# Performance work log

Hardware: AMD Instinct MI355X
Metric: run time of the kernel (lower is better)

The kernel has to match this reference:

```python
import jax, jax.numpy as jnp
import numpy as np

B, T, S0 = 8, 4, 4096
D_MODEL, H, D, R, RANK = 2048, 16, 128, 64, 512
C = D - R  # content dim = 64


def _rope(x, positions):
    # x: [B, H, T, R]; rotate-half style RoPE as in the torch module
    half = x.shape[-1] // 2
    inv_freq = 1.0 / (10000.0 ** (jnp.arange(half, dtype=jnp.float32) / half))
    freqs = positions.astype(jnp.float32)[:, None] * inv_freq[None, :]  # [T, half]
    cos = jnp.cos(freqs)[None, None].astype(x.dtype)
    sin = jnp.sin(freqs)[None, None].astype(x.dtype)
    x1, x2 = x[..., :half], x[..., half:]
    return jnp.concatenate([x1 * cos - x2 * sin, x1 * sin + x2 * cos], axis=-1)


def setup_inputs() -> dict:
    key = jax.random.key(0)
    ks = jax.random.split(key, 9)
    s = 0.02
    return {
        "x": jax.random.normal(ks[0], (B, T, D_MODEL), jnp.float32),
        "cache_c_kv": jax.random.normal(ks[1], (B, S0, RANK), jnp.float32),
        "cache_k_rope": jax.random.normal(ks[2], (B, S0, H, R), jnp.float32),
        "w_q": jax.random.normal(ks[3], (D_MODEL, H * C), jnp.float32) * s,
        "w_q_rope": jax.random.normal(ks[4], (D_MODEL, H * R), jnp.float32) * s,
        "w_kv_down": jax.random.normal(ks[5], (D_MODEL, RANK), jnp.float32) * s,
        "w_kv_up": jax.random.normal(ks[6], (RANK, H * D), jnp.float32) * s,
        "w_k_rope": jax.random.normal(ks[7], (D_MODEL, H * R), jnp.float32) * s,
        "w_out": jax.random.normal(ks[8], (H * D, D_MODEL), jnp.float32) * s,
    }


def reference(x, cache_c_kv, cache_k_rope, w_q, w_q_rope, w_kv_down, w_kv_up, w_k_rope, w_out):
    cache_len = cache_c_kv.shape[1]
    positions = jnp.arange(cache_len, cache_len + T)

    # queries
    q_content = (x @ w_q).reshape(B, T, H, C).transpose(0, 2, 1, 3)        # [B,H,T,C]
    q_rope = (x @ w_q_rope).reshape(B, T, H, R).transpose(0, 2, 1, 3)      # [B,H,T,R]
    q_rope = _rope(q_rope, positions)
    q = jnp.concatenate([q_content, q_rope], axis=-1)                       # [B,H,T,D]

    # new compressed kv + rope keys, append to cache
    c_kv_new = x @ w_kv_down                                                # [B,T,RANK]
    k_rope_new = (x @ w_k_rope).reshape(B, T, H, R).transpose(0, 2, 1, 3)
    k_rope_new = _rope(k_rope_new, positions).transpose(0, 2, 1, 3)         # [B,T,H,R]
    c_kv = jnp.concatenate([cache_c_kv, c_kv_new], axis=1)                  # [B,S,RANK]
    k_rope = jnp.concatenate([cache_k_rope, k_rope_new], axis=1)            # [B,S,H,R]

    # decompress full cache every step (the expensive MLA pattern)
    S = c_kv.shape[1]
    kv = (c_kv @ w_kv_up).reshape(B, S, H, D)                               # [B,S,H,D]
    k_content = kv[..., :C].transpose(0, 2, 1, 3)                           # [B,H,S,C]
    v = kv.transpose(0, 2, 1, 3)                                            # [B,H,S,D]
    k = jnp.concatenate([k_content, k_rope.transpose(0, 2, 1, 3)], axis=-1) # [B,H,S,D]

    # kv_cache present => is_prefill False => no causal mask (faithful to source)
    scale = 1.0 / jnp.sqrt(jnp.asarray(D, dtype=q.dtype))
    scores = jnp.einsum('bhtd,bhsd->bhts', q, k) * scale
    attn = jax.nn.softmax(scores, axis=-1)
    out = jnp.einsum('bhts,bhsd->bhtd', attn, v)                            # [B,H,T,D]
    out = out.transpose(0, 2, 1, 3).reshape(B, T, H * D)
    return out @ w_out                                                       # [B,T,D_MODEL]
```

## Files before the change

### kernel.cpp

```cpp
#include <hip/hip_runtime.h>
#include <hip/hip_fp16.h>
#include <cmath>

#define BB 8
#define TT 4
#define HH 16
#define DDIM 128
#define RRDIM 64
#define CCDIM 64
#define RANKC 512
#define DMODEL 2048
#define S0C 4096
#define NQ 64
#define HD 2048
#define NACT 3584
#define NSC 65
#define SPAD 4160
#define SCALE_ATT 0.08838834764831845f
#define LP 72
#define OLP 136

typedef __attribute__((ext_vector_type(8))) short bf16x8;
typedef __attribute__((ext_vector_type(4))) float f32x4;
typedef unsigned short ushortT;

#define AIDX(row, kk) ((row)*132 + (((row)>>2)<<2) + (kk))

static __device__ __forceinline__ unsigned short f2bf(float x) {
  unsigned u = __float_as_uint(x);
  u += 0x7FFFu + ((u >> 16) & 1u);
  return (unsigned short)(u >> 16);
}
static __device__ __forceinline__ float bf2f(unsigned v16) {
  return __uint_as_float(v16 << 16);
}
static __device__ __forceinline__ unsigned pk2(float a, float b) {
  return (unsigned)f2bf(a) | ((unsigned)f2bf(b) << 16);
}

__global__ __launch_bounds__(256) void k_front(const float* __restrict__ A,
                                               const float* __restrict__ w0,
                                               const float* __restrict__ w1,
                                               const float* __restrict__ w2,
                                               const float* __restrict__ w3,
                                               const float* __restrict__ cckv,
                                               float* __restrict__ part,
                                               ushortT* __restrict__ ckvT) {
  __shared__ float shf[4352];
  const int tid = threadIdx.x;
  const int bx = blockIdx.x;
  if (bx < 448) {
    const int cb = bx % 28;
    const int k0 = (bx / 28) * 128;
    const float* W; int N, lc0, off;
    if (cb < 8)       { W = w0; N = 1024; lc0 = cb * 128;        off = 0; }
    else if (cb < 16) { W = w1; N = 1024; lc0 = (cb - 8) * 128;  off = 1024; }
    else if (cb < 20) { W = w2; N = 512;  lc0 = (cb - 16) * 128; off = 2048; }
    else              { W = w3; N = 1024; lc0 = (cb - 20) * 128; off = 2560; }
    {
      const int row = tid >> 3;
      const int kseg = (tid & 7) * 16;
      const float4* s4 = reinterpret_cast<const float4*>(A + (size_t)row * DMODEL + k0 + kseg);
      float4 v0 = s4[0], v1 = s4[1], v2 = s4[2], v3 = s4[3];
      *reinterpret_cast<float4*>(&shf[AIDX(row, kseg)])      = v0;
      *reinterpret_cast<float4*>(&shf[AIDX(row, kseg + 4)])  = v1;
      *reinterpret_cast<float4*>(&shf[AIDX(row, kseg + 8)])  = v2;
      *reinterpret_cast<float4*>(&shf[AIDX(row, kseg + 12)]) = v3;
    }
    __syncthreads();
    const int cg = tid & 31;
    const int rg = tid >> 5;
    float acc[4][4];
    #pragma unroll
    for (int r = 0; r < 4; ++r)
      #pragma unroll
      for (int c = 0; c < 4; ++c) acc[r][c] = 0.f;
    #pragma unroll 4
    for (int kk = 0; kk < 128; ++kk) {
      const float4 w4 = *reinterpret_cast<const float4*>(W + (size_t)(k0 + kk) * N + lc0 + cg * 4);
      const float wv[4] = {w4.x, w4.y, w4.z, w4.w};
      #pragma unroll
      for (int r = 0; r < 4; ++r) {
        const float av = shf[AIDX(rg * 4 + r, kk)];
        #pragma unroll
        for (int c = 0; c < 4; ++c) acc[r][c] = fmaf(av, wv[c], acc[r][c]);
      }
    }
    #pragma unroll
    for (int r = 0; r < 4; ++r) {
      float4 o = make_float4(acc[r][0], acc[r][1], acc[r][2], acc[r][3]);
      *reinterpret_cast<float4*>(part + ((size_t)(bx / 28) * 32 + rg * 4 + r) * NACT + off + lc0 + cg * 4) = o;
    }
  } else if (bx < 960) {
    ushortT* tlds = reinterpret_cast<ushortT*>(shf);
    const int idx = bx - 448;
    const int b = idx >> 6, c = idx & 63;
    const float* src = cckv + ((size_t)b * S0C + c * 64) * RANKC;
    ushortT* dstT = ckvT + ((size_t)(b * NSC + c) * RANKC) * 64;
    const int s = tid >> 2, rq = tid & 3;
    const int rloc = tid >> 1, shalf = (tid & 1) * 32;
    for (int slab = 0; slab < 4; ++slab) {
      const int r0 = slab * 128;
      #pragma unroll
      for (int i = 0; i < 8; ++i) {
        const float4 v = *reinterpret_cast<const float4*>(src + (size_t)s * RANKC + r0 + rq * 32 + i * 4);
        *reinterpret_cast<uint2*>(&tlds[s * 136 + rq * 32 + i * 4]) =
            make_uint2(pk2(v.x, v.y), pk2(v.z, v.w));
      }
      __syncthreads();
      alignas(16) ushortT a[32];
      #pragma unroll
      for (int j = 0; j < 32; ++j) a[j] = tlds[(shalf + j) * 136 + rloc];
      uint4* d = reinterpret_cast<uint4*>(dstT + ((size_t)(r0 + rloc)) * 64 + shalf);
      const uint4* ap = reinterpret_cast<const uint4*>(a);
      d[0] = ap[0]; d[1] = ap[1]; d[2] = ap[2]; d[3] = ap[3];
      __syncthreads();
    }
  } else {
    const int b = bx - 960;
    uint4* p = reinterpret_cast<uint4*>(ckvT + ((size_t)(b * NSC + 64) * RANKC) * 64);
    const uint4 z = make_uint4(0, 0, 0, 0);
    for (int i = tid; i < 2048; i += 256) p[i] = z;
  }
}

__global__ __launch_bounds__(256) void k_proj(const float* __restrict__ A,
                                              const float* __restrict__ W,
                                              float* __restrict__ part,
                                              int N, int NTOT, int coloff) {
  __shared__ float a_lds[4352];
  const int tid = threadIdx.x;
  const int c0 = blockIdx.x * 128;
  const int k0 = blockIdx.y * 128;
  {
    const int row = tid >> 3;
    const int kseg = (tid & 7) * 16;
    const float4* s4 = reinterpret_cast<const float4*>(A + (size_t)row * DMODEL + k0 + kseg);
    float4 v0 = s4[0], v1 = s4[1], v2 = s4[2], v3 = s4[3];
    *reinterpret_cast<float4*>(&a_lds[AIDX(row, kseg)])      = v0;
    *reinterpret_cast<float4*>(&a_lds[AIDX(row, kseg + 4)])  = v1;
    *reinterpret_cast<float4*>(&a_lds[AIDX(row, kseg + 8)])  = v2;
    *reinterpret_cast<float4*>(&a_lds[AIDX(row, kseg + 12)]) = v3;
  }
  __syncthreads();
  const int cg = tid & 31;
  const int rg = tid >> 5;
  float acc[4][4];
  #pragma unroll
  for (int r = 0; r < 4; ++r)
    #pragma unroll
    for (int c = 0; c < 4; ++c) acc[r][c] = 0.f;
  #pragma unroll 4
  for (int kk = 0; kk < 128; ++kk) {
    const float4 w4 = *reinterpret_cast<const float4*>(W + (size_t)(k0 + kk) * N + c0 + cg * 4);
    const float wv[4] = {w4.x, w4.y, w4.z, w4.w};
    #pragma unroll
    for (int r = 0; r < 4; ++r) {
      const float av = a_lds[AIDX(rg * 4 + r, kk)];
      #pragma unroll
      for (int c = 0; c < 4; ++c) acc[r][c] = fmaf(av, wv[c], acc[r][c]);
    }
  }
  #pragma unroll
  for (int r = 0; r < 4; ++r) {
    float4 o = make_float4(acc[r][0], acc[r][1], acc[r][2], acc[r][3]);
    *reinterpret_cast<float4*>(part + ((size_t)blockIdx.y * 32 + rg * 4 + r) * NTOT + coloff + c0 + cg * 4) = o;
  }
}

__global__ __launch_bounds__(256) void k_reduce(const float* __restrict__ part,
                                                float* __restrict__ out, int total, int nsplit) {
  int g = blockIdx.x * 256 + threadIdx.x;
  if (g >= total) return;
  float s = 0.f;
  #pragma unroll 4
  for (int c = 0; c < nsplit; ++c) s += part[(size_t)c * total + g];
  out[g] = s;
}

__global__ __launch_bounds__(256) void k_qlatrope(const float* __restrict__ act,
                                                  const float* __restrict__ wup,
                                                  ushortT* __restrict__ qlat,
                                                  float* __restrict__ qrope,
                                                  float* __restrict__ ckvn,
                                                  float* __restrict__ krn,
                                                  ushortT* __restrict__ ckvT) {
  __shared__ float wt[64 * 132];
  __shared__ float a_s[32 * 68];
  const int tid = threadIdx.x;
  const int bx = blockIdx.x;
  if (bx < 64) {
    const int h = bx & 15;
    const int r0 = (bx >> 4) * 128;
    {
      const int r = tid >> 1;
      const int cseg = (tid & 1) * 32;
      const float* src = wup + (size_t)(r0 + r) * HD + h * DDIM + cseg;
      #pragma unroll
      for (int u = 0; u < 8; ++u) {
        const float4 v = *reinterpret_cast<const float4*>(src + u * 4);
        wt[(cseg + u * 4 + 0) * 132 + r] = v.x;
        wt[(cseg + u * 4 + 1) * 132 + r] = v.y;
        wt[(cseg + u * 4 + 2) * 132 + r] = v.z;
        wt[(cseg + u * 4 + 3) * 132 + r] = v.w;
      }
    }
    {
      const int bt = tid >> 3;
      const int cseg = (tid & 7) * 8;
      const float4* s4 = reinterpret_cast<const float4*>(act + (size_t)bt * NACT + h * CCDIM + cseg);
      float4 v0 = s4[0], v1 = s4[1];
      *reinterpret_cast<float4*>(&a_s[bt * 68 + cseg])     = v0;
      *reinterpret_cast<float4*>(&a_s[bt * 68 + cseg + 4]) = v1;
    }
    __syncthreads();
    const int r = tid & 127;
    const int bth = tid >> 7;
    float acc[16];
    #pragma unroll
    for (int i = 0; i < 16; ++i) acc[i] = 0.f;
    #pragma unroll 8
    for (int c = 0; c < 64; ++c) {
      const float wv = wt[c * 132 + r];
      #pragma unroll
      for (int i = 0; i < 16; ++i)
        acc[i] = fmaf(a_s[(bth * 16 + i) * 68 + c], wv, acc[i]);
    }
    #pragma unroll
    for (int i = 0; i < 16; ++i) {
      const int bt = bth * 16 + i;
      const int b = bt >> 2, t = bt & 3;
      qlat[((size_t)(b * NQ) + h * TT + t) * RANKC + r0 + r] = f2bf(acc[i]);
    }
    return;
  }
  int g = (bx - 64) * 256 + tid;
  if (g < BB * TT * HH * 32) {
    const int hj = g & 31;
    const int h = (g >> 5) & 15;
    const int t = (g >> 9) & 3;
    const int b = g >> 11;
    const float* arow = act + (size_t)(b * TT + t) * NACT + 1024 + h * RRDIM;
    const float x1 = arow[hj], x2 = arow[hj + 32];
    const double fr = (double)(S0C + t) * pow(10000.0, -(double)hj / 32.0);
    const float cs = (float)cos(fr), sn = (float)sin(fr);
    const int qi = h * TT + t;
    qrope[((size_t)b * NQ + qi) * RRDIM + hj]      = x1 * cs - x2 * sn;
    qrope[((size_t)b * NQ + qi) * RRDIM + hj + 32] = x1 * sn + x2 * cs;
    return;
  }
  g -= BB * TT * HH * 32;
  if (g < BB * TT * HH * 32) {
    const int hj = g & 31;
    const int h = (g >> 5) & 15;
    const int t = (g >> 9) & 3;
    const int b = g >> 11;
    const float* arow = act + (size_t)(b * TT + t) * NACT + 2560 + h * RRDIM;
    const float x1 = arow[hj], x2 = arow[hj + 32];
    const double fr = (double)(S0C + t) * pow(10000.0, -(double)hj / 32.0);
    const float cs = (float)cos(fr), sn = (float)sin(fr);
    krn[((size_t)(b * TT + t) * HH + h) * RRDIM + hj]      = x1 * cs - x2 * sn;
    krn[((size_t)(b * TT + t) * HH + h) * RRDIM + hj + 32] = x1 * sn + x2 * cs;
    return;
  }
  g -= BB * TT * HH * 32;
  if (g < BB * TT * RANKC) {
    const int r = g & 511;
    const int bt = g >> 9;
    const int b = bt >> 2, t = bt & 3;
    const float v = act[(size_t)bt * NACT + 2048 + r];
    ckvn[g] = v;
    ckvT[(((size_t)(b * NSC + 64) * RANKC) + r) * 64 + t] = f2bf(v);
  }
}

__global__ __launch_bounds__(256) void k_rscore(const float* __restrict__ cache_kr,
                                                const float* __restrict__ krn,
                                                const float* __restrict__ qrope,
                                                __half* __restrict__ rs) {
  const int bh = blockIdx.x;
  const int b = bh >> 4, h = bh & 15;
  const int tid = threadIdx.x;
  const int ql = tid & 3;
  float4 qf[4][4];
  const float* qrb = qrope + ((size_t)b * NQ + h * TT) * RRDIM;
  #pragma unroll
  for (int t = 0; t < 4; ++t)
    #pragma unroll
    for (int u = 0; u < 4; ++u)
      qf[t][u] = *reinterpret_cast<const float4*>(qrb + t * RRDIM + ql * 16 + u * 4);
  const int s0 = blockIdx.y * 512;
  #pragma unroll 1
  for (int pass = 0; pass < 8; ++pass) {
    const int s = s0 + pass * 64 + (tid >> 2);
    if (s < 4100) {
      const float* krow = (s < S0C)
        ? cache_kr + (((size_t)b * S0C + s) * HH + h) * RRDIM
        : krn + (((size_t)b * TT + (s - S0C)) * HH + h) * RRDIM;
      float p[4] = {0.f, 0.f, 0.f, 0.f};
      #pragma unroll
      for (int u = 0; u < 4; ++u) {
        const float4 kv = *reinterpret_cast<const float4*>(krow + ql * 16 + u * 4);
        #pragma unroll
        for (int t = 0; t < 4; ++t) {
          p[t] += kv.x * qf[t][u].x + kv.y * qf[t][u].y
                + kv.z * qf[t][u].z + kv.w * qf[t][u].w;
        }
      }
      #pragma unroll
      for (int t = 0; t < 4; ++t) {
        p[t] += __shfl_xor(p[t], 1, 4);
        p[t] += __shfl_xor(p[t], 2, 4);
      }
      rs[((size_t)bh * 4 + ql) * SPAD + s] = __float2half(p[ql] * SCALE_ATT);
    }
  }
}

__global__ __launch_bounds__(256) void k_attn(
    const float* __restrict__ cache_ckv, const float* __restrict__ ckvn,
    const ushortT* __restrict__ qlat, const ushortT* __restrict__ ckvT,
    const __half* __restrict__ rs, float* __restrict__ ml,
    ushortT* __restrict__ olat) {
  __shared__ ushortT smem[23040];
  ushortT* const QA0 = smem;
  ushortT* const QA1 = smem + 4608;
  ushortT* const KB0 = smem + 9216;
  ushortT* const KB1 = smem + 13824;
  ushortT* const CT  = smem;
  ushortT* const OL  = smem + 9216;
  ushortT* const PL  = smem + 18432;

  const int tid = threadIdx.x;
  const int lane = tid & 63;
  const int wv = tid >> 6;
  const int m0 = wv * 16;
  const int lm = lane & 15;
  const int lg = lane >> 4;
  const int b = blockIdx.x, chunk = blockIdx.y;
  const int scnt = (chunk < 64) ? 64 : TT;
  const float* bsrc = (chunk < 64)
      ? cache_ckv + ((size_t)b * S0C + (size_t)chunk * 64) * RANKC
      : ckvn + (size_t)b * TT * RANKC;
  const ushortT* qsrc = qlat + (size_t)b * NQ * RANKC;

  float rv[4][4];
  #pragma unroll
  for (int reg = 0; reg < 4; ++reg) {
    const int q = m0 + lg * 4 + reg;
    const __half* rp = rs + ((size_t)(b * HH + (q >> 2)) * TT + (q & 3)) * SPAD + chunk * 64;
    #pragma unroll
    for (int st = 0; st < 4; ++st)
      rv[reg][st] = __half2float(rp[st * 16 + lm]);
  }

  const int srow = tid >> 2;
  const int rseg = (tid & 3) * 16;
  uint4 qreg[2];
  float4 kreg[4];
  auto loadStageA = [&](int kt) {
    const uint4* qp = reinterpret_cast<const uint4*>(qsrc + (size_t)srow * RANKC + kt * 64 + rseg);
    qreg[0] = qp[0]; qreg[1] = qp[1];
    if (srow < scnt) {
      const float4* kp = reinterpret_cast<const float4*>(bsrc + (size_t)srow * RANKC + kt * 64 + rseg);
      kreg[0] = kp[0]; kreg[1] = kp[1]; kreg[2] = kp[2]; kreg[3] = kp[3];
    } else {
      kreg[0] = make_float4(0.f, 0.f, 0.f, 0.f); kreg[1] = kreg[0]; kreg[2] = kreg[0]; kreg[3] = kreg[0];
    }
  };
  auto writeStageA = [&](ushortT* qa, ushortT* kb) {
    *reinterpret_cast<uint4*>(&qa[srow * LP + rseg])     = qreg[0];
    *reinterpret_cast<uint4*>(&qa[srow * LP + rseg + 8]) = qreg[1];
    *reinterpret_cast<uint4*>(&kb[srow * LP + rseg]) =
        make_uint4(pk2(kreg[0].x, kreg[0].y), pk2(kreg[0].z, kreg[0].w),
                   pk2(kreg[1].x, kreg[1].y), pk2(kreg[1].z, kreg[1].w));
    *reinterpret_cast<uint4*>(&kb[srow * LP + rseg + 8]) =
        make_uint4(pk2(kreg[2].x, kreg[2].y), pk2(kreg[2].z, kreg[2].w),
                   pk2(kreg[3].x, kreg[3].y), pk2(kreg[3].z, kreg[3].w));
  };

  f32x4 acc[4];
  #pragma unroll
  for (int st = 0; st < 4; ++st) acc[st] = (f32x4){0.f, 0.f, 0.f, 0.f};

  loadStageA(0);
  writeStageA(QA0, KB0);
  loadStageA(1);
  __syncthreads();
  for (int kt = 0; kt < 8; ++kt) {
    if (kt < 7) {
      writeStageA((kt & 1) ? QA0 : QA1, (kt & 1) ? KB0 : KB1);
      if (kt < 6) loadStageA(kt + 2);
    }
    const ushortT* qa = (kt & 1) ? QA1 : QA0;
    const ushortT* kb = (kt & 1) ? KB1 : KB0;
    #pragma unroll
    for (int ks = 0; ks < 2; ++ks) {
      const bf16x8 af = *reinterpret_cast<const bf16x8*>(&qa[(m0 + lm) * LP + ks * 32 + lg * 8]);
      #pragma unroll
      for (int st = 0; st < 4; ++st) {
        const bf16x8 bfv = *reinterpret_cast<const bf16x8*>(&kb[(st * 16 + lm) * LP + ks * 32 + lg * 8]);
        acc[st] = __builtin_amdgcn_mfma_f32_16x16x32_bf16(af, bfv, acc[st], 0, 0, 0);
      }
    }
    __syncthreads();
  }

  const ushortT* ctsrc = ckvT + ((size_t)(b * NSC + chunk) * RANKC) * 64;
  const int rloc = tid >> 1;
  const int shalf = (tid & 1) * 32;
  uint4 creg[4];
  auto loadCT = [&](int rg) {
    const uint4* p = reinterpret_cast<const uint4*>(ctsrc + ((size_t)(rg * 128 + rloc)) * 64 + shalf);
    creg[0] = p[0]; creg[1] = p[1]; creg[2] = p[2]; creg[3] = p[3];
  };
  auto writeCT = [&]() {
    uint4* d = reinterpret_cast<uint4*>(&CT[rloc * LP + shalf]);
    d[0] = creg[0]; d[1] = creg[1]; d[2] = creg[2]; d[3] = creg[3];
  };
  loadCT(0);

  #pragma unroll
  for (int reg = 0; reg < 4; ++reg) {
    const int q = m0 + lg * 4 + reg;
    float vv[4];
    float mx = -1e30f;
    #pragma unroll
    for (int st = 0; st < 4; ++st) {
      const int sl = st * 16 + lm;
      const float val = (sl < scnt) ? fmaf(acc[st][reg], SCALE_ATT, rv[reg][st]) : -1e30f;
      vv[st] = val;
      mx = fmaxf(mx, val);
    }
    #pragma unroll
    for (int off = 1; off < 16; off <<= 1) mx = fmaxf(mx, __shfl_xor(mx, off, 16));
    float sum = 0.f;
    #pragma unroll
    for (int st = 0; st < 4; ++st) {
      const float p = __expf(vv[st] - mx);
      vv[st] = p;
      sum += p;
    }
    #pragma unroll
    for (int off = 1; off < 16; off <<= 1) sum += __shfl_xor(sum, off, 16);
    #pragma unroll
    for (int st = 0; st < 4; ++st)
      PL[q * LP + st * 16 + lm] = f2bf(vv[st]);
    if (lm == 0) {
      const size_t mb = (((size_t)b * NSC + chunk) * NQ + q) * 2;
      ml[mb] = mx; ml[mb + 1] = sum;
    }
  }
  __syncthreads();

  writeCT();
  loadCT(1);
  const bf16x8 pa0 = *reinterpret_cast<const bf16x8*>(&PL[(m0 + lm) * LP + lg * 8]);
  const bf16x8 pa1 = *reinterpret_cast<const bf16x8*>(&PL[(m0 + lm) * LP + 32 + lg * 8]);
  __syncthreads();

  const size_t obase = ((size_t)(b * NSC + chunk) * NQ) * RANKC;
  for (int rg = 0; rg < 4; ++rg) {
    f32x4 a2[8];
    #pragma unroll
    for (int nt = 0; nt < 8; ++nt) a2[nt] = (f32x4){0.f, 0.f, 0.f, 0.f};
    #pragma unroll
    for (int nt = 0; nt < 8; ++nt) {
      const bf16x8 b0 = *reinterpret_cast<const bf16x8*>(&CT[(nt * 16 + lm) * LP + lg * 8]);
      const bf16x8 b1 = *reinterpret_cast<const bf16x8*>(&CT[(nt * 16 + lm) * LP + 32 + lg * 8]);
      a2[nt] = __builtin_amdgcn_mfma_f32_16x16x32_bf16(pa0, b0, a2[nt], 0, 0, 0);
      a2[nt] = __builtin_amdgcn_mfma_f32_16x16x32_bf16(pa1, b1, a2[nt], 0, 0, 0);
    }
    #pragma unroll
    for (int nt = 0; nt < 8; ++nt)
      #pragma unroll
      for (int reg = 0; reg < 4; ++reg)
        OL[(m0 + lg * 4 + reg) * OLP + nt * 16 + lm] = f2bf(a2[nt][reg]);
    __syncthreads();
    {
      const int q = tid >> 2;
      const int seg = (tid & 3) * 32;
      const uint4* s4 = reinterpret_cast<const uint4*>(&OL[q * OLP + seg]);
      uint4* d4 = reinterpret_cast<uint4*>(&olat[obase + (size_t)q * RANKC + rg * 128 + seg]);
      d4[0] = s4[0]; d4[1] = s4[1]; d4[2] = s4[2]; d4[3] = s4[3];
    }
    if (rg < 3) {
      writeCT();
      if (rg < 2) loadCT(rg + 2);
      __syncthreads();
    }
  }
}

__global__ __launch_bounds__(512) void k_combF(const float* __restrict__ ml,
                                               const ushortT* __restrict__ olat,
                                               const float* __restrict__ wup,
                                               float* __restrict__ ohead) {
  __shared__ float wrow[4][66];
  __shared__ float att_lds[4][516];
  const int h = blockIdx.x, b = blockIdx.y;
  const int tid = threadIdx.x;
  const int wave = tid >> 6;
  const int i = wave >> 1;
  const int rhalf = wave & 1;
  const int rl = tid & 63;
  const int qi = h * TT + i;
  float m1 = -1e30f, l1 = 0.f, m2 = -1e30f, l2 = 0.f;
  {
    const size_t base = (((size_t)b * NSC + rl) * NQ + qi) * 2;
    m1 = ml[base]; l1 = ml[base + 1];
    if (rl == 0) {
      const size_t b2 = (((size_t)b * NSC + 64) * NQ + qi) * 2;
      m2 = ml[b2]; l2 = ml[b2 + 1];
    }
  }
  float M = fmaxf(m1, m2);
  #pragma unroll
  for (int off = 1; off < 64; off <<= 1) M = fmaxf(M, __shfl_xor(M, off));
  float L = l1 * __expf(m1 - M) + ((rl == 0) ? l2 * __expf(m2 - M) : 0.f);
  #pragma unroll
  for (int off = 1; off < 64; off <<= 1) L += __shfl_xor(L, off);
  const float invL = 1.0f / L;
  wrow[i][rl] = __expf(m1 - M) * invL;
  if (rl == 0) wrow[i][64] = __expf(m2 - M) * invL;
  __syncthreads();
  const int r0 = rhalf * 256 + rl * 4;
  float o0 = 0.f, o1 = 0.f, o2 = 0.f, o3 = 0.f;
  for (int c = 0; c < NSC; ++c) {
    const float w = wrow[i][c];
    const uint2 v = *reinterpret_cast<const uint2*>(
        olat + (((size_t)b * NSC + c) * NQ + qi) * RANKC + r0);
    o0 = fmaf(bf2f(v.x & 0xffffu), w, o0);
    o1 = fmaf(bf2f(v.x >> 16), w, o1);
    o2 = fmaf(bf2f(v.y & 0xffffu), w, o2);
    o3 = fmaf(bf2f(v.y >> 16), w, o3);
  }
  *reinterpret_cast<float4*>(&att_lds[i][r0]) = make_float4(o0, o1, o2, o3);
  __syncthreads();
  const int col = tid & 127;
  const int t = tid >> 7;
  float acc = 0.f;
  #pragma unroll 8
  for (int r = 0; r < RANKC; ++r)
    acc = fmaf(att_lds[t][r], wup[(size_t)r * HD + h * DDIM + col], acc);
  ohead[(size_t)(b * TT + t) * HD + h * DDIM + col] = acc;
}

extern "C" void kernel_launch(void* const* d_in, const int* in_sizes, int n_in,
                              void* d_out, int out_size, void* d_ws, size_t ws_size,
                              hipStream_t stream) {
  const float* x     = (const float*)d_in[0];
  const float* cckv  = (const float*)d_in[1];
  const float* ckr   = (const float*)d_in[2];
  const float* w_q   = (const float*)d_in[3];
  const float* w_qr  = (const float*)d_in[4];
  const float* w_kvd = (const float*)d_in[5];
  const float* w_kvu = (const float*)d_in[6];
  const float* w_kr  = (const float*)d_in[7];
  const float* w_out = (const float*)d_in[8];
  float* out = (float*)d_out;
  float* ws = (float*)d_ws;

  size_t off = 0;
  float* act      = ws + off; off += 32ull * NACT;
  ushortT* qlat   = (ushortT*)(ws + off); off += 131072;
  float* qrope    = ws + off; off += 32768;
  float* ckvn     = ws + off; off += 16384;
  float* krn      = ws + off; off += 32768;
  float* mlb      = ws + off; off += (size_t)BB * NSC * NQ * 2;
  float* ohead    = ws + off; off += 65536;
  __half* rsb     = (__half*)(ws + off); off += 1064960;
  ushortT* ckvT   = (ushortT*)(ws + off); off += 8519680;
  float* regB  = ws + off;
  float* part0 = regB;
  ushortT* olat = (ushortT*)regB;
  float* part3 = regB;

  k_front<<<dim3(968), 256, 0, stream>>>(x, w_q, w_qr, w_kvd, w_kr, cckv, part0, ckvT);
  k_reduce<<<dim3(448), 256, 0, stream>>>(part0, act, 32 * NACT, 16);
  k_qlatrope<<<dim3(256), 256, 0, stream>>>(act, w_kvu, qlat, qrope, ckvn, krn, ckvT);
  k_rscore<<<dim3(128, 9), 256, 0, stream>>>(ckr, krn, qrope, rsb);

  k_attn<<<dim3(BB, NSC), 256, 0, stream>>>(cckv, ckvn, qlat, ckvT, rsb, mlb, olat);

  k_combF<<<dim3(16, 8), 512, 0, stream>>>(mlb, olat, w_kvu, ohead);
  k_proj<<<dim3(16, 16), 256, 0, stream>>>(ohead, w_out, part3, 2048, 2048, 0);
  k_reduce<<<dim3(256), 256, 0, stream>>>(part3, out, 32 * HD, 16);
}
```

Measured before the change: 241.6 us.

## Split latent attention into score and grouped PV kernels with in-register chunk merging

The fused attention kernel is split into a score kernel that writes softmax probabilities to global memory and a PV kernel. The PV kernel merges four sequence chunks per block in registers using per-chunk max/sum rescaling, so the partial output buffer has 17 groups in fp32 instead of 65 chunks in bf16, which shrinks what the combine kernel reads. The PV work is also spread over four rank slices per block, giving more blocks. In exchange the probabilities make an extra global round trip and a third launch is added. The transpose writer is reworked to pack pairs of bf16 into words, and the zero-fill of the padded chunk is widened to cover all of it.

```diff
diff --git a/kernel.cpp b/kernel.cpp
--- a/kernel.cpp
+++ b/kernel.cpp
@@ -15,10 +15,10 @@
 #define HD 2048
 #define NACT 3584
 #define NSC 65
+#define NG 17
 #define SPAD 4160
 #define SCALE_ATT 0.08838834764831845f
 #define LP 72
-#define OLP 136
 
 typedef __attribute__((ext_vector_type(8))) short bf16x8;
 typedef __attribute__((ext_vector_type(4))) float f32x4;
@@ -108,19 +108,25 @@
             make_uint2(pk2(v.x, v.y), pk2(v.z, v.w));
       }
       __syncthreads();
-      alignas(16) ushortT a[32];
-      #pragma unroll
-      for (int j = 0; j < 32; ++j) a[j] = tlds[(shalf + j) * 136 + rloc];
+      unsigned wv[16];
+      #pragma unroll
+      for (int k = 0; k < 16; ++k) {
+        const unsigned t0 = tlds[(shalf + 2 * k)     * 136 + rloc];
+        const unsigned t1 = tlds[(shalf + 2 * k + 1) * 136 + rloc];
+        wv[k] = t0 | (t1 << 16);
+      }
       uint4* d = reinterpret_cast<uint4*>(dstT + ((size_t)(r0 + rloc)) * 64 + shalf);
-      const uint4* ap = reinterpret_cast<const uint4*>(a);
-      d[0] = ap[0]; d[1] = ap[1]; d[2] = ap[2]; d[3] = ap[3];
+      d[0] = make_uint4(wv[0], wv[1], wv[2], wv[3]);
+      d[1] = make_uint4(wv[4], wv[5], wv[6], wv[7]);
+      d[2] = make_uint4(wv[8], wv[9], wv[10], wv[11]);
+      d[3] = make_uint4(wv[12], wv[13], wv[14], wv[15]);
       __syncthreads();
     }
   } else {
     const int b = bx - 960;
     uint4* p = reinterpret_cast<uint4*>(ckvT + ((size_t)(b * NSC + 64) * RANKC) * 64);
     const uint4 z = make_uint4(0, 0, 0, 0);
-    for (int i = tid; i < 2048; i += 256) p[i] = z;
+    for (int i = tid; i < 4096; i += 256) p[i] = z;
   }
 }
 
@@ -317,20 +323,16 @@
   }
 }
 
-__global__ __launch_bounds__(256) void k_attn(
-    const float* __restrict__ cache_ckv, const float* __restrict__ ckvn,
-    const ushortT* __restrict__ qlat, const ushortT* __restrict__ ckvT,
-    const __half* __restrict__ rs, float* __restrict__ ml,
-    ushortT* __restrict__ olat) {
+__global__ __launch_bounds__(256) void k_score(
+    const float* __restrict__ cckv, const float* __restrict__ ckvn,
+    const ushortT* __restrict__ qlat, const __half* __restrict__ rs,
+    float* __restrict__ ml, ushortT* __restrict__ Pg) {
   __shared__ ushortT smem[23040];
   ushortT* const QA0 = smem;
   ushortT* const QA1 = smem + 4608;
   ushortT* const KB0 = smem + 9216;
   ushortT* const KB1 = smem + 13824;
-  ushortT* const CT  = smem;
-  ushortT* const OL  = smem + 9216;
   ushortT* const PL  = smem + 18432;
-
   const int tid = threadIdx.x;
   const int lane = tid & 63;
   const int wv = tid >> 6;
@@ -340,25 +342,15 @@
   const int b = blockIdx.x, chunk = blockIdx.y;
   const int scnt = (chunk < 64) ? 64 : TT;
   const float* bsrc = (chunk < 64)
-      ? cache_ckv + ((size_t)b * S0C + (size_t)chunk * 64) * RANKC
+      ? cckv + ((size_t)b * S0C + (size_t)chunk * 64) * RANKC
       : ckvn + (size_t)b * TT * RANKC;
   const ushortT* qsrc = qlat + (size_t)b * NQ * RANKC;
-
-  float rv[4][4];
-  #pragma unroll
-  for (int reg = 0; reg < 4; ++reg) {
-    const int q = m0 + lg * 4 + reg;
-    const __half* rp = rs + ((size_t)(b * HH + (q >> 2)) * TT + (q & 3)) * SPAD + chunk * 64;
-    #pragma unroll
-    for (int st = 0; st < 4; ++st)
-      rv[reg][st] = __half2float(rp[st * 16 + lm]);
-  }
 
   const int srow = tid >> 2;
   const int rseg = (tid & 3) * 16;
   uint4 qreg[2];
   float4 kreg[4];
-  auto loadStageA = [&](int kt) {
+  auto loadA = [&](int kt) {
     const uint4* qp = reinterpret_cast<const uint4*>(qsrc + (size_t)srow * RANKC + kt * 64 + rseg);
     qreg[0] = qp[0]; qreg[1] = qp[1];
     if (srow < scnt) {
@@ -368,7 +360,7 @@
       kreg[0] = make_float4(0.f, 0.f, 0.f, 0.f); kreg[1] = kreg[0]; kreg[2] = kreg[0]; kreg[3] = kreg[0];
     }
   };
-  auto writeStageA = [&](ushortT* qa, ushortT* kb) {
+  auto writeA = [&](ushortT* qa, ushortT* kb) {
     *reinterpret_cast<uint4*>(&qa[srow * LP + rseg])     = qreg[0];
     *reinterpret_cast<uint4*>(&qa[srow * LP + rseg + 8]) = qreg[1];
     *reinterpret_cast<uint4*>(&kb[srow * LP + rseg]) =
@@ -383,14 +375,14 @@
   #pragma unroll
   for (int st = 0; st < 4; ++st) acc[st] = (f32x4){0.f, 0.f, 0.f, 0.f};
 
-  loadStageA(0);
-  writeStageA(QA0, KB0);
-  loadStageA(1);
+  loadA(0);
+  writeA(QA0, KB0);
+  loadA(1);
   __syncthreads();
   for (int kt = 0; kt < 8; ++kt) {
     if (kt < 7) {
-      writeStageA((kt & 1) ? QA0 : QA1, (kt & 1) ? KB0 : KB1);
-      if (kt < 6) loadStageA(kt + 2);
+      writeA((kt & 1) ? QA0 : QA1, (kt & 1) ? KB0 : KB1);
+      if (kt < 6) loadA(kt + 2);
     }
     const ushortT* qa = (kt & 1) ? QA1 : QA0;
     const ushortT* kb = (kt & 1) ? KB1 : KB0;
@@ -406,29 +398,18 @@
     __syncthreads();
   }
 
-  const ushortT* ctsrc = ckvT + ((size_t)(b * NSC + chunk) * RANKC) * 64;
-  const int rloc = tid >> 1;
-  const int shalf = (tid & 1) * 32;
-  uint4 creg[4];
-  auto loadCT = [&](int rg) {
-    const uint4* p = reinterpret_cast<const uint4*>(ctsrc + ((size_t)(rg * 128 + rloc)) * 64 + shalf);
-    creg[0] = p[0]; creg[1] = p[1]; creg[2] = p[2]; creg[3] = p[3];
-  };
-  auto writeCT = [&]() {
-    uint4* d = reinterpret_cast<uint4*>(&CT[rloc * LP + shalf]);
-    d[0] = creg[0]; d[1] = creg[1]; d[2] = creg[2]; d[3] = creg[3];
-  };
-  loadCT(0);
-
   #pragma unroll
   for (int reg = 0; reg < 4; ++reg) {
     const int q = m0 + lg * 4 + reg;
+    const __half* rp = rs + ((size_t)(b * HH + (q >> 2)) * TT + (q & 3)) * SPAD + chunk * 64;
     float vv[4];
     float mx = -1e30f;
     #pragma unroll
     for (int st = 0; st < 4; ++st) {
       const int sl = st * 16 + lm;
-      const float val = (sl < scnt) ? fmaf(acc[st][reg], SCALE_ATT, rv[reg][st]) : -1e30f;
+      const float val = (sl < scnt)
+          ? fmaf(acc[st][reg], SCALE_ATT, __half2float(rp[st * 16 + lm]))
+          : -1e30f;
       vv[st] = val;
       mx = fmaxf(mx, val);
     }
@@ -453,14 +434,86 @@
   }
   __syncthreads();
 
-  writeCT();
-  loadCT(1);
-  const bf16x8 pa0 = *reinterpret_cast<const bf16x8*>(&PL[(m0 + lm) * LP + lg * 8]);
-  const bf16x8 pa1 = *reinterpret_cast<const bf16x8*>(&PL[(m0 + lm) * LP + 32 + lg * 8]);
+  {
+    const int prow = tid >> 2;
+    const int pseg = (tid & 3) * 16;
+    const uint4* sp = reinterpret_cast<const uint4*>(&PL[prow * LP + pseg]);
+    uint4* dp = reinterpret_cast<uint4*>(Pg + ((size_t)(b * NSC + chunk) * NQ + prow) * 64 + pseg);
+    dp[0] = sp[0]; dp[1] = sp[1];
+  }
+}
+
+__global__ __launch_bounds__(256) void k_pv(
+    const ushortT* __restrict__ ckvT, const ushortT* __restrict__ Pg,
+    const float* __restrict__ ml, float* __restrict__ olat,
+    float* __restrict__ mlg) {
+  __shared__ ushortT CT[128 * LP];
+  __shared__ ushortT PLs[64 * LP];
+  __shared__ float wlds[4][68];
+  const int tid = threadIdx.x;
+  const int lane = tid & 63;
+  const int wv = tid >> 6;
+  const int m0 = wv * 16;
+  const int lm = lane & 15;
+  const int lg = lane >> 4;
+  const int b = blockIdx.x, g = blockIdx.y, rg = blockIdx.z;
+  const int nc = (g < 16) ? 4 : 1;
+  const int c0 = (g < 16) ? g * 4 : 64;
+
+  if (lm == 0) {
+    #pragma unroll
+    for (int reg = 0; reg < 4; ++reg) {
+      const int q = m0 + lg * 4 + reg;
+      float mg = -1e30f;
+      for (int c = 0; c < nc; ++c)
+        mg = fmaxf(mg, ml[(((size_t)b * NSC + c0 + c) * NQ + q) * 2]);
+      float la = 0.f;
+      for (int c = 0; c < nc; ++c) {
+        const size_t mb = (((size_t)b * NSC + c0 + c) * NQ + q) * 2;
+        const float w = __expf(ml[mb] - mg);
+        la = fmaf(ml[mb + 1], w, la);
+        wlds[c][q] = w;
+      }
+      if (blockIdx.z == 0) {
+        const size_t gb = (((size_t)b * NG + g) * NQ + q) * 2;
+        mlg[gb] = mg; mlg[gb + 1] = la;
+      }
+    }
+  }
+
+  const int rloc = tid >> 1;
+  const int shalf = (tid & 1) * 32;
+  const int prow = tid >> 2;
+  const int pseg = (tid & 3) * 16;
+  uint4 ctreg[4];
+  uint4 plreg[2];
+  auto loadc = [&](int c) {
+    const uint4* cp = reinterpret_cast<const uint4*>(
+        ckvT + (((size_t)(b * NSC + c0 + c) * RANKC) + rg * 128 + rloc) * 64 + shalf);
+    ctreg[0] = cp[0]; ctreg[1] = cp[1]; ctreg[2] = cp[2]; ctreg[3] = cp[3];
+    const uint4* pp = reinterpret_cast<const uint4*>(
+        Pg + ((size_t)(b * NSC + c0 + c) * NQ + prow) * 64 + pseg);
+    plreg[0] = pp[0]; plreg[1] = pp[1];
+  };
+  auto writec = [&]() {
+    uint4* d = reinterpret_cast<uint4*>(&CT[rloc * LP + shalf]);
+    d[0] = ctreg[0]; d[1] = ctreg[1]; d[2] = ctreg[2]; d[3] = ctreg[3];
+    uint4* p = reinterpret_cast<uint4*>(&PLs[prow * LP + pseg]);
+    p[0] = plreg[0]; p[1] = plreg[1];
+  };
+
+  f32x4 OACC[8];
+  #pragma unroll
+  for (int nt = 0; nt < 8; ++nt) OACC[nt] = (f32x4){0.f, 0.f, 0.f, 0.f};
+
+  loadc(0);
   __syncthreads();
-
-  const size_t obase = ((size_t)(b * NSC + chunk) * NQ) * RANKC;
-  for (int rg = 0; rg < 4; ++rg) {
+  for (int c = 0; c < nc; ++c) {
+    writec();
+    __syncthreads();
+    if (c + 1 < nc) loadc(c + 1);
+    const bf16x8 pa0 = *reinterpret_cast<const bf16x8*>(&PLs[(m0 + lm) * LP + lg * 8]);
+    const bf16x8 pa1 = *reinterpret_cast<const bf16x8*>(&PLs[(m0 + lm) * LP + 32 + lg * 8]);
     f32x4 a2[8];
     #pragma unroll
     for (int nt = 0; nt < 8; ++nt) a2[nt] = (f32x4){0.f, 0.f, 0.f, 0.f};
@@ -471,32 +524,26 @@
       a2[nt] = __builtin_amdgcn_mfma_f32_16x16x32_bf16(pa0, b0, a2[nt], 0, 0, 0);
       a2[nt] = __builtin_amdgcn_mfma_f32_16x16x32_bf16(pa1, b1, a2[nt], 0, 0, 0);
     }
-    #pragma unroll
-    for (int nt = 0; nt < 8; ++nt)
-      #pragma unroll
-      for (int reg = 0; reg < 4; ++reg)
-        OL[(m0 + lg * 4 + reg) * OLP + nt * 16 + lm] = f2bf(a2[nt][reg]);
+    const f32x4 w = (f32x4){wlds[c][m0 + lg * 4 + 0], wlds[c][m0 + lg * 4 + 1],
+                            wlds[c][m0 + lg * 4 + 2], wlds[c][m0 + lg * 4 + 3]};
+    #pragma unroll
+    for (int nt = 0; nt < 8; ++nt) OACC[nt] += w * a2[nt];
     __syncthreads();
-    {
-      const int q = tid >> 2;
-      const int seg = (tid & 3) * 32;
-      const uint4* s4 = reinterpret_cast<const uint4*>(&OL[q * OLP + seg]);
-      uint4* d4 = reinterpret_cast<uint4*>(&olat[obase + (size_t)q * RANKC + rg * 128 + seg]);
-      d4[0] = s4[0]; d4[1] = s4[1]; d4[2] = s4[2]; d4[3] = s4[3];
-    }
-    if (rg < 3) {
-      writeCT();
-      if (rg < 2) loadCT(rg + 2);
-      __syncthreads();
-    }
-  }
-}
-
-__global__ __launch_bounds__(512) void k_combF(const float* __restrict__ ml,
-                                               const ushortT* __restrict__ olat,
+  }
+
+  const size_t obase = ((size_t)(b * NG + g) * NQ) * RANKC;
+  #pragma unroll
+  for (int nt = 0; nt < 8; ++nt)
+    #pragma unroll
+    for (int reg = 0; reg < 4; ++reg)
+      olat[obase + (size_t)(m0 + lg * 4 + reg) * RANKC + rg * 128 + nt * 16 + lm] = OACC[nt][reg];
+}
+
+__global__ __launch_bounds__(512) void k_combF(const float* __restrict__ mlg,
+                                               const float* __restrict__ olat,
                                                const float* __restrict__ wup,
                                                float* __restrict__ ohead) {
-  __shared__ float wrow[4][66];
+  __shared__ float wrow[4][20];
   __shared__ float att_lds[4][516];
   const int h = blockIdx.x, b = blockIdx.y;
   const int tid = threadIdx.x;
@@ -505,35 +552,28 @@
   const int rhalf = wave & 1;
   const int rl = tid & 63;
   const int qi = h * TT + i;
-  float m1 = -1e30f, l1 = 0.f, m2 = -1e30f, l2 = 0.f;
-  {
-    const size_t base = (((size_t)b * NSC + rl) * NQ + qi) * 2;
-    m1 = ml[base]; l1 = ml[base + 1];
-    if (rl == 0) {
-      const size_t b2 = (((size_t)b * NSC + 64) * NQ + qi) * 2;
-      m2 = ml[b2]; l2 = ml[b2 + 1];
-    }
-  }
-  float M = fmaxf(m1, m2);
+  float m1 = -1e30f, l1 = 0.f;
+  if (rl < NG) {
+    const size_t base = (((size_t)b * NG + rl) * NQ + qi) * 2;
+    m1 = mlg[base]; l1 = mlg[base + 1];
+  }
+  float M = m1;
   #pragma unroll
   for (int off = 1; off < 64; off <<= 1) M = fmaxf(M, __shfl_xor(M, off));
-  float L = l1 * __expf(m1 - M) + ((rl == 0) ? l2 * __expf(m2 - M) : 0.f);
+  float L = (rl < NG) ? l1 * __expf(m1 - M) : 0.f;
   #pragma unroll
   for (int off = 1; off < 64; off <<= 1) L += __shfl_xor(L, off);
   const float invL = 1.0f / L;
-  wrow[i][rl] = __expf(m1 - M) * invL;
-  if (rl == 0) wrow[i][64] = __expf(m2 - M) * invL;
+  if (rl < NG) wrow[i][rl] = __expf(m1 - M) * invL;
   __syncthreads();
   const int r0 = rhalf * 256 + rl * 4;
   float o0 = 0.f, o1 = 0.f, o2 = 0.f, o3 = 0.f;
-  for (int c = 0; c < NSC; ++c) {
+  for (int c = 0; c < NG; ++c) {
     const float w = wrow[i][c];
-    const uint2 v = *reinterpret_cast<const uint2*>(
-        olat + (((size_t)b * NSC + c) * NQ + qi) * RANKC + r0);
-    o0 = fmaf(bf2f(v.x & 0xffffu), w, o0);
-    o1 = fmaf(bf2f(v.x >> 16), w, o1);
-    o2 = fmaf(bf2f(v.y & 0xffffu), w, o2);
-    o3 = fmaf(bf2f(v.y >> 16), w, o3);
+    const float4 v = *reinterpret_cast<const float4*>(
+        olat + (((size_t)b * NG + c) * NQ + qi) * RANKC + r0);
+    o0 = fmaf(v.x, w, o0); o1 = fmaf(v.y, w, o1);
+    o2 = fmaf(v.z, w, o2); o3 = fmaf(v.w, w, o3);
   }
   *reinterpret_cast<float4*>(&att_lds[i][r0]) = make_float4(o0, o1, o2, o3);
   __syncthreads();
@@ -568,12 +608,14 @@
   float* ckvn     = ws + off; off += 16384;
   float* krn      = ws + off; off += 32768;
   float* mlb      = ws + off; off += (size_t)BB * NSC * NQ * 2;
+  float* mlgb     = ws + off; off += (size_t)BB * NG * NQ * 2;
   float* ohead    = ws + off; off += 65536;
   __half* rsb     = (__half*)(ws + off); off += 1064960;
   ushortT* ckvT   = (ushortT*)(ws + off); off += 8519680;
+  ushortT* Pgb    = (ushortT*)(ws + off); off += 1064960;
   float* regB  = ws + off;
   float* part0 = regB;
-  ushortT* olat = (ushortT*)regB;
+  float* olat  = regB;
   float* part3 = regB;
 
   k_front<<<dim3(968), 256, 0, stream>>>(x, w_q, w_qr, w_kvd, w_kr, cckv, part0, ckvT);
@@ -581,9 +623,10 @@
   k_qlatrope<<<dim3(256), 256, 0, stream>>>(act, w_kvu, qlat, qrope, ckvn, krn, ckvT);
   k_rscore<<<dim3(128, 9), 256, 0, stream>>>(ckr, krn, qrope, rsb);
 
-  k_attn<<<dim3(BB, NSC), 256, 0, stream>>>(cckv, ckvn, qlat, ckvT, rsb, mlb, olat);
-
-  k_combF<<<dim3(16, 8), 512, 0, stream>>>(mlb, olat, w_kvu, ohead);
+  k_score<<<dim3(BB, NSC), 256, 0, stream>>>(cckv, ckvn, qlat, rsb, mlb, Pgb);
+  k_pv<<<dim3(BB, NG, 4), 256, 0, stream>>>(ckvT, Pgb, mlb, olat, mlgb);
+
+  k_combF<<<dim3(16, 8), 512, 0, stream>>>(mlgb, olat, w_kvu, ohead);
   k_proj<<<dim3(16, 16), 256, 0, stream>>>(ohead, w_out, part3, 2048, 2048, 0);
   k_reduce<<<dim3(256), 256, 0, stream>>>(part3, out, 32 * HD, 16);
 }
```

Result: faster. 235.8 us (-2.4%).
